# Optimization experiments

Hardware: AMD Instinct MI355X
Metric: run time of the kernel (lower is better)

The kernel has to match this reference:

```python
import jax, jax.numpy as jnp
import numpy as np

B, S, E, H, Dh = 2, 2048, 1024, 16, 64


def setup_inputs() -> dict:
    key = jax.random.key(0)
    ks = jax.random.split(key, 8)
    w = 0.02
    return {
        "x": jax.random.normal(ks[0], (B, S, E), jnp.float32),
        # torch Linear convention: weight (out, in) = (Dh, E), stacked over heads
        "Wq": jax.random.normal(ks[1], (H, Dh, E), jnp.float32) * w,
        "bq": jax.random.normal(ks[2], (H, Dh), jnp.float32) * w,
        "Wk": jax.random.normal(ks[3], (H, Dh, E), jnp.float32) * w,
        "bk": jax.random.normal(ks[4], (H, Dh), jnp.float32) * w,
        "Wv": jax.random.normal(ks[5], (H, Dh, E), jnp.float32) * w,
        "bv": jax.random.normal(ks[6], (H, Dh), jnp.float32) * w,
        "proj": jax.random.normal(ks[7], (H * Dh, E), jnp.float32) * w,
    }


def reference(x, Wq, bq, Wk, bk, Wv, bv, proj):
    b, s, e = x.shape
    h, dh, _ = Wq.shape
    scale = jnp.sqrt(jnp.asarray(dh, x.dtype))
    # per-head linear projections: y = x @ W.T + b  -> (b, h, s, dh)
    q = jnp.einsum('bse,hde->bhsd', x, Wq) + bq[None, :, None, :]
    k = jnp.einsum('bse,hde->bhsd', x, Wk) + bk[None, :, None, :]
    v = jnp.einsum('bse,hde->bhsd', x, Wv) + bv[None, :, None, :]
    causal = jnp.triu(jnp.ones((s, s), bool), 1)
    scores = jnp.einsum('bhsd,bhtd->bhst', q, k) / scale
    scores = jnp.where(causal[None, None], -jnp.inf, scores)
    # quirk: softmax output divided by sqrt(head_size) a second time
    att = jax.nn.softmax(scores, axis=-1) / scale
    z = jnp.einsum('bhst,bhtd->bhsd', att, v)
    # quirk: torch reshapes (B,H,S,Dh) row-major into (B,S,H*Dh) WITHOUT transpose
    z = z.reshape(b, s, h * dh)
    return z @ proj
```

## Files before the change

### kernel.cpp

```cpp
#include <hip/hip_runtime.h>
#include <hip/hip_bf16.h>

typedef unsigned short u16;
typedef unsigned int u32;
typedef __bf16 bf16x8 __attribute__((ext_vector_type(8)));
typedef float f32x4 __attribute__((ext_vector_type(4)));
typedef u16 u16x8 __attribute__((ext_vector_type(8)));
typedef u16 u16x4 __attribute__((ext_vector_type(4)));
typedef u32 u32x4 __attribute__((ext_vector_type(4)));

#define B_ 2
#define S_ 2048
#define E_ 1024
#define H_ 16
#define Dh_ 64

static __device__ __forceinline__ u16 f2bf(float f) {
  unsigned u = __builtin_bit_cast(unsigned, f);
  u += 0x7fff + ((u >> 16) & 1);
  return (u16)(u >> 16);
}

static __device__ __forceinline__ void gload16(const u16* g, u16* l) {
  __builtin_amdgcn_global_load_lds((const __attribute__((address_space(1))) unsigned int*)g,
                                   (__attribute__((address_space(3))) unsigned int*)l,
                                   16, 0, 0);
}

__global__ void cvt_all(const float* __restrict__ x, const float* __restrict__ wq,
                        const float* __restrict__ wk, const float* __restrict__ wv,
                        u16* __restrict__ xb, u16* __restrict__ wcat) {
  const int i = blockIdx.x * 256 + threadIdx.x;
  const float* src; u16x8* dst;
  if (i < 524288) {
    src = x + (size_t)i * 8;            dst = (u16x8*)xb + i;
  } else {
    const int j = i - 524288;
    dst = (u16x8*)wcat + j;
    if (j < 131072)      src = wq + (size_t)j * 8;
    else if (j < 262144) src = wk + (size_t)(j - 131072) * 8;
    else                 src = wv + (size_t)(j - 262144) * 8;
  }
  float4 a = ((const float4*)src)[0], b = ((const float4*)src)[1];
  u16x8 o;
  o[0] = f2bf(a.x); o[1] = f2bf(a.y); o[2] = f2bf(a.z); o[3] = f2bf(a.w);
  o[4] = f2bf(b.x); o[5] = f2bf(b.y); o[6] = f2bf(b.z); o[7] = f2bf(b.w);
  *dst = o;
}

__global__ void transpose_cvt(const float* __restrict__ in, u16* __restrict__ outT) {
  __shared__ float t[32][33];
  const int e = blockIdx.x * 32 + threadIdx.x;
  const int f = blockIdx.y * 32 + threadIdx.y;
  t[threadIdx.y][threadIdx.x] = in[f * 1024 + e];
  __syncthreads();
  const int eo = blockIdx.x * 32 + threadIdx.y;
  const int fo = blockIdx.y * 32 + threadIdx.x;
  outT[eo * 1024 + fo] = f2bf(t[threadIdx.x][threadIdx.y]);
}

__global__ __launch_bounds__(512, 2) void qkv_gemm(const u16* __restrict__ Wcat,
                                                   const u16* __restrict__ Xm,
                                                   const float* __restrict__ bq,
                                                   const float* __restrict__ bk,
                                                   const float* __restrict__ bv,
                                                   u16* __restrict__ Qb, u16* __restrict__ Kb,
                                                   u16* __restrict__ Vtb, float qs) {
  __shared__ __align__(16) u16 Alds[2][16384];
  __shared__ __align__(16) u16 Blds[2][16384];
  const int tid = threadIdx.x;
  const int wv = tid >> 6, ln = tid & 63;
  const int lq = ln & 15, lg = ln >> 4;
  const int wm = wv >> 2, wn = wv & 3;
  const int bid = blockIdx.x;
  const int xcd = bid & 7, w = bid >> 3;
  const int bx = w % 12;
  const int by = xcd * 2 + w / 12;
  const int ra0 = bx * 256, rb0 = by * 256;

  const int r_t = tid >> 3, c_t = tid & 7;
  const int gcol = (c_t ^ (r_t & 7)) * 8;
  const u16* Asrc = Wcat + (ra0 + r_t) * 1024 + gcol;
  const u16* Bsrc = Xm   + (rb0 + r_t) * 1024 + gcol;

  const int sc0 = (lg ^ (lq & 7)) * 8;
  const int sc1 = ((4 + lg) ^ (lq & 7)) * 8;
  const int baseA = (wm * 128 + lq) * 64;
  const int baseB = (wn * 64 + lq) * 64;

  f32x4 acc[8][4];
  const f32x4 z4 = {0.f, 0.f, 0.f, 0.f};
#pragma unroll
  for (int i = 0; i < 8; ++i)
#pragma unroll
    for (int j = 0; j < 4; ++j) acc[i][j] = z4;

#define SA(Q, KT, BUF) gload16(Asrc + (Q) * 65536 + (KT) * 64, &Alds[BUF][((Q) * 512 + tid) * 8])
#define SB(Q, KT, BUF) gload16(Bsrc + (Q) * 65536 + (KT) * 64, &Blds[BUF][((Q) * 512 + tid) * 8])
#define LOADA(MH, SC) do {                                                         \
    _Pragma("unroll") for (int ii = 0; ii < 4; ++ii)                               \
      af[ii] = *(const bf16x8*)&Alds[cb][baseA + (MH) * 4096 + ii * 1024 + (SC)];  \
  } while (0)
#define LOADB(DST, SC) do {                                                        \
    _Pragma("unroll") for (int j = 0; j < 4; ++j)                                  \
      DST[j] = *(const bf16x8*)&Blds[cb][baseB + j * 1024 + (SC)];                 \
  } while (0)
#define MF(MH, BQ) do {                                                            \
    _Pragma("unroll") for (int ii = 0; ii < 4; ++ii)                               \
      _Pragma("unroll") for (int j = 0; j < 4; ++j)                                \
        acc[(MH) * 4 + ii][j] =                                                    \
            __builtin_amdgcn_mfma_f32_16x16x32_bf16(af[ii], BQ[j],                 \
                                                    acc[(MH) * 4 + ii][j], 0, 0, 0); \
  } while (0)

  SB(0, 0, 0); SB(1, 0, 0); SB(2, 0, 0); SB(3, 0, 0);
  SA(0, 0, 0); SA(2, 0, 0); SA(1, 0, 0); SA(3, 0, 0);

  for (int kt = 0; kt < 16; ++kt) {
    const int cb = kt & 1, nb = cb ^ 1;
    const bool st = (kt < 15);
    asm volatile("s_waitcnt vmcnt(2)" ::: "memory");
    __builtin_amdgcn_s_barrier();
    __builtin_amdgcn_sched_barrier(0);
    bf16x8 af[4], bq0[4], bq1[4];
    LOADA(0, sc0);
    LOADB(bq0, sc0);
    if (st) { SB(0, kt + 1, nb); SB(1, kt + 1, nb); }
    __builtin_amdgcn_s_barrier();
    asm volatile("s_waitcnt lgkmcnt(0)" ::: "memory");
    __builtin_amdgcn_sched_barrier(0);
    __builtin_amdgcn_s_setprio(1);
    MF(0, bq0);
    __builtin_amdgcn_s_setprio(0);
    __builtin_amdgcn_s_barrier();
    LOADA(0, sc1);
    LOADB(bq1, sc1);
    if (st) { SB(2, kt + 1, nb); SB(3, kt + 1, nb); }
    __builtin_amdgcn_s_barrier();
    asm volatile("s_waitcnt lgkmcnt(0)" ::: "memory");
    __builtin_amdgcn_sched_barrier(0);
    __builtin_amdgcn_s_setprio(1);
    MF(0, bq1);
    __builtin_amdgcn_s_setprio(0);
    __builtin_amdgcn_s_barrier();
    if (st) { asm volatile("s_waitcnt vmcnt(4)" ::: "memory"); }
    else    { asm volatile("s_waitcnt vmcnt(0)" ::: "memory"); }
    __builtin_amdgcn_s_barrier();
    __builtin_amdgcn_sched_barrier(0);
    LOADA(1, sc0);
    if (st) { SA(0, kt + 1, nb); SA(2, kt + 1, nb); }
    __builtin_amdgcn_s_barrier();
    asm volatile("s_waitcnt lgkmcnt(0)" ::: "memory");
    __builtin_amdgcn_sched_barrier(0);
    __builtin_amdgcn_s_setprio(1);
    MF(1, bq0);
    __builtin_amdgcn_s_setprio(0);
    __builtin_amdgcn_s_barrier();
    LOADA(1, sc1);
    if (st) { SA(1, kt + 1, nb); SA(3, kt + 1, nb); }
    __builtin_amdgcn_s_barrier();
    asm volatile("s_waitcnt lgkmcnt(0)" ::: "memory");
    __builtin_amdgcn_sched_barrier(0);
    __builtin_amdgcn_s_setprio(1);
    MF(1, bq1);
    __builtin_amdgcn_s_setprio(0);
    __builtin_amdgcn_s_barrier();
  }
#undef SA
#undef SB
#undef LOADA
#undef LOADB
#undef MF

  const int region = bx >> 2;
  const float* bias = (region == 0) ? bq : (region == 1) ? bk : bv;
  const float osc = (region == 0) ? qs : 1.0f;
#pragma unroll
  for (int i = 0; i < 8; ++i) {
#pragma unroll
    for (int j = 0; j < 4; ++j) {
      const int n0 = ra0 + wm * 128 + (i >> 2) * 64 + (i & 3) * 16 + lg * 4;
      const int nl = n0 & 1023;
      const int h = nl >> 6, d = nl & 63;
      const int m = rb0 + wn * 64 + j * 16 + lq;
      const int bb = m >> 11, s = m & 2047;
      const float4 b4 = *(const float4*)&bias[nl];
      if (region < 2) {
        u16* out = (region == 0) ? Qb : Kb;
        u16x4 pk;
        pk[0] = f2bf((acc[i][j][0] + b4.x) * osc);
        pk[1] = f2bf((acc[i][j][1] + b4.y) * osc);
        pk[2] = f2bf((acc[i][j][2] + b4.z) * osc);
        pk[3] = f2bf((acc[i][j][3] + b4.w) * osc);
        *(u16x4*)&out[((bb * H_ + h) * S_ + s) * Dh_ + d] = pk;
      } else {
        const float bvv[4] = {b4.x, b4.y, b4.z, b4.w};
#pragma unroll
        for (int r = 0; r < 4; ++r)
          Vtb[((bb * H_ + h) * Dh_ + d + r) * S_ + s] = f2bf(acc[i][j][r] + bvv[r]);
      }
    }
  }
}

__global__ __launch_bounds__(256) void proj_gemm(const u16* __restrict__ Am,
                                                 const u16* __restrict__ Bm,
                                                 float* __restrict__ out) {
  __shared__ __align__(16) u16 As[2][4096];
  __shared__ __align__(16) u16 Bs[2][2048];
  const int tid = threadIdx.x;
  const int wv = tid >> 6, ln = tid & 63;
  const int lq = ln & 15, lg = ln >> 4;
  const int bid = blockIdx.x;
  const int xcd = bid & 7, within = bid >> 3;
  const int bx = within & 7;
  const int by = xcd * 8 + (within >> 3);
  const int ra0 = bx * 128, rb0 = by * 64;
  const int wra = wv >> 1, wrb = wv & 1;

  f32x4 acc[4][2];
  const f32x4 z4 = {0.f, 0.f, 0.f, 0.f};
#pragma unroll
  for (int i = 0; i < 4; ++i)
#pragma unroll
    for (int j = 0; j < 2; ++j) acc[i][j] = z4;

  const int arow = tid >> 2;
  const int acol = (tid & 3) * 8;
  const int brow = wv * 16 + (ln >> 2);
  const int bcol = (ln & 3) * 8;
  const u16* Ags = Am + (ra0 + arow) * 1024 + acol;
  const u16* Bgs = Bm + (rb0 + brow) * 1024 + bcol;

#define PSTAGE(KT, BUF) do { const int k0_ = (KT) * 32;              \
    gload16(Ags + k0_,         &As[BUF][wv * 512]);                  \
    gload16(Ags + 65536 + k0_, &As[BUF][wv * 512 + 2048]);           \
    gload16(Bgs + k0_,         &Bs[BUF][wv * 512]); } while (0)

  PSTAGE(0, 0);
  for (int kt = 0; kt < 32; ++kt) {
    const int cb = kt & 1;
    if (kt < 31) {
      PSTAGE(kt + 1, cb ^ 1);
      asm volatile("s_waitcnt vmcnt(3)" ::: "memory");
    } else {
      asm volatile("s_waitcnt vmcnt(0)" ::: "memory");
    }
    __builtin_amdgcn_s_barrier();
    __builtin_amdgcn_sched_barrier(0);
    bf16x8 af[4], bfr[2];
#pragma unroll
    for (int i = 0; i < 4; ++i)
      af[i] = *(const bf16x8*)&As[cb][(wra * 64 + i * 16 + lq) * 32 + lg * 8];
#pragma unroll
    for (int j = 0; j < 2; ++j)
      bfr[j] = *(const bf16x8*)&Bs[cb][(wrb * 32 + j * 16 + lq) * 32 + lg * 8];
#pragma unroll
    for (int i = 0; i < 4; ++i)
#pragma unroll
      for (int j = 0; j < 2; ++j)
        acc[i][j] = __builtin_amdgcn_mfma_f32_16x16x32_bf16(af[i], bfr[j], acc[i][j], 0, 0, 0);
    __builtin_amdgcn_sched_barrier(0);
    __builtin_amdgcn_s_barrier();
  }
#undef PSTAGE

  const int Ar = ra0 + wra * 64, Br = rb0 + wrb * 32;
#pragma unroll
  for (int i = 0; i < 4; ++i)
#pragma unroll
    for (int j = 0; j < 2; ++j) {
      const int e0 = Ar + i * 16 + lg * 4;
      const int m = Br + j * 16 + lq;
      *(f32x4*)&out[m * 1024 + e0] = acc[i][j];
    }
}

__global__ __launch_bounds__(512, 4) void attn_kernel(const u16* __restrict__ Q,
                                                      const u16* __restrict__ K,
                                                      const u16* __restrict__ Vt,
                                                      u16* __restrict__ Z) {
  __shared__ __align__(16) u16 Ktile[2][8192];
  __shared__ __align__(16) u16 Vtile[2][8192];
  const int tid = threadIdx.x;
  const int wv = tid >> 6, ln = tid & 63;
  const int lq = ln & 15, lg = ln >> 4;
  const bool lgodd = (lg & 1) != 0;
  const int id = blockIdx.x;
  const int within = id >> 3;
  const int xg = id & 7;
  int bh, qt;
  if (within < 32) { bh = xg * 4 + (within >> 4);     qt = 15 - (within & 15); }
  else { const int w = within - 32; bh = xg * 4 + 2 + (w >> 4); qt = w & 15; }
  const int qrow = (qt << 7) + wv * 16 + lq;
  const u16* Qp = Q + (size_t)bh * S_ * Dh_;
  const u16* Kp = K + (size_t)bh * S_ * Dh_;
  const u16* Vp = Vt + (size_t)bh * Dh_ * S_;

  int kgofs[2], vgrow[2], vgcol[2];
#pragma unroll
  for (int j = 0; j < 2; ++j) {
    const int p = j * 512 + tid;
    const int gk = p ^ ((p >> 3) & 7);
    kgofs[j] = (gk >> 3) * 64 + (gk & 7) * 8;
    vgrow[j] = p >> 4;
    vgcol[j] = ((p & 15) ^ ((p >> 4) & 15)) * 8;
  }
  const int sc0 = (lg ^ (lq & 7)) * 8;
  const int sc1 = ((4 + lg) ^ (lq & 7)) * 8;

  bf16x8 qf0 = *(const bf16x8*)&Qp[qrow * Dh_ + lg * 8];
  bf16x8 qf1 = *(const bf16x8*)&Qp[qrow * Dh_ + 32 + lg * 8];

  f32x4 o[4];
  const f32x4 z4 = {0.f, 0.f, 0.f, 0.f};
#pragma unroll
  for (int dt = 0; dt < 4; ++dt) o[dt] = z4;
  float l_lane = 0.f;

#define STAGE(KT, BUF) do { const int kb_ = (KT) * 128;                              \
    gload16(Kp + (size_t)kb_ * 64 + kgofs[0], &Ktile[BUF][wv * 512]);                \
    gload16(Kp + (size_t)kb_ * 64 + kgofs[1], &Ktile[BUF][4096 + wv * 512]);         \
    gload16(Vp + (size_t)vgrow[0] * 2048 + kb_ + vgcol[0], &Vtile[BUF][wv * 512]);   \
    gload16(Vp + (size_t)vgrow[1] * 2048 + kb_ + vgcol[1], &Vtile[BUF][4096 + wv * 512]); \
  } while (0)

  STAGE(0, 0);

  int cur = 0;
  for (int kt = 0; kt <= qt; ++kt) {
    if (kt < qt) {
      STAGE(kt + 1, cur ^ 1);
      asm volatile("s_waitcnt vmcnt(4)" ::: "memory");
    } else {
      asm volatile("s_waitcnt vmcnt(0)" ::: "memory");
    }
    __builtin_amdgcn_s_barrier();
    __builtin_amdgcn_sched_barrier(0);
    const int k0 = kt * 128;
    const bool diag = (kt == qt);
    const int nkk = diag ? ((wv >> 1) + 1) : 4;
#pragma unroll
    for (int kk = 0; kk < 4; ++kk) {
      if (kk < nkk) {
        const int rA = (kk * 32 + lq) * 64;
        const int rB = rA + 1024;
        bf16x8 kA0 = *(const bf16x8*)&Ktile[cur][rA + sc0];
        bf16x8 kA1 = *(const bf16x8*)&Ktile[cur][rA + sc1];
        bf16x8 kB0 = *(const bf16x8*)&Ktile[cur][rB + sc0];
        bf16x8 kB1 = *(const bf16x8*)&Ktile[cur][rB + sc1];
        f32x4 sa = z4, sb = z4;
        __builtin_amdgcn_s_setprio(1);
        sa = __builtin_amdgcn_mfma_f32_16x16x32_bf16(kA0, qf0, sa, 0, 0, 0);
        sa = __builtin_amdgcn_mfma_f32_16x16x32_bf16(kA1, qf1, sa, 0, 0, 0);
        sb = __builtin_amdgcn_mfma_f32_16x16x32_bf16(kB0, qf0, sb, 0, 0, 0);
        sb = __builtin_amdgcn_mfma_f32_16x16x32_bf16(kB1, qf1, sb, 0, 0, 0);
        __builtin_amdgcn_s_setprio(0);
        if (diag) {
          const int keyA = k0 + kk * 32 + lg * 4;
          const int keyB = keyA + 16;
#pragma unroll
          for (int r = 0; r < 4; ++r) {
            if (keyA + r > qrow) sa[r] = -3.0e38f;
            if (keyB + r > qrow) sb[r] = -3.0e38f;
          }
        }
        float e0 = __builtin_amdgcn_exp2f(sa[0]);
        float e1 = __builtin_amdgcn_exp2f(sa[1]);
        float e2 = __builtin_amdgcn_exp2f(sa[2]);
        float e3 = __builtin_amdgcn_exp2f(sa[3]);
        float f0 = __builtin_amdgcn_exp2f(sb[0]);
        float f1 = __builtin_amdgcn_exp2f(sb[1]);
        float f2 = __builtin_amdgcn_exp2f(sb[2]);
        float f3 = __builtin_amdgcn_exp2f(sb[3]);
        l_lane += ((e0 + e1) + (e2 + e3)) + ((f0 + f1) + (f2 + f3));
        u32 A0, A1, B0, B1;
        asm("v_cvt_pk_bf16_f32 %0, %1, %2" : "=v"(A0) : "v"(e0), "v"(e1));
        asm("v_cvt_pk_bf16_f32 %0, %1, %2" : "=v"(A1) : "v"(e2), "v"(e3));
        asm("v_cvt_pk_bf16_f32 %0, %1, %2" : "=v"(B0) : "v"(f0), "v"(f1));
        asm("v_cvt_pk_bf16_f32 %0, %1, %2" : "=v"(B1) : "v"(f2), "v"(f3));
        asm("v_permlane32_swap_b32 %0, %1" : "+v"(A0), "+v"(B0));
        asm("v_permlane32_swap_b32 %0, %1" : "+v"(A1), "+v"(B1));
        const u32 A0x = __shfl_xor((int)A0, 16), B0x = __shfl_xor((int)B0, 16);
        const u32 A1x = __shfl_xor((int)A1, 16), B1x = __shfl_xor((int)B1, 16);
        u32x4 w;
        w[0] = lgodd ? B0x : A0;
        w[1] = lgodd ? B1x : A1;
        w[2] = lgodd ? B0 : A0x;
        w[3] = lgodd ? B1 : A1x;
        const bf16x8 pf = __builtin_bit_cast(bf16x8, w);
        const int scvk = ((kk * 4 + lg) ^ lq) * 8;
        __builtin_amdgcn_s_setprio(1);
#pragma unroll
        for (int dt = 0; dt < 4; ++dt) {
          bf16x8 vf = *(const bf16x8*)&Vtile[cur][(dt * 16 + lq) * 128 + scvk];
          o[dt] = __builtin_amdgcn_mfma_f32_16x16x32_bf16(vf, pf, o[dt], 0, 0, 0);
        }
        __builtin_amdgcn_s_setprio(0);
      }
    }
    __builtin_amdgcn_sched_barrier(0);
    __builtin_amdgcn_s_barrier();
    cur ^= 1;
  }
#undef STAGE

  float l = l_lane;
  l += __shfl_xor(l, 16);
  l += __shfl_xor(l, 32);
  const float inv = 0.125f / l;
#pragma unroll
  for (int dt = 0; dt < 4; ++dt) {
    u16x4 pko;
#pragma unroll
    for (int r = 0; r < 4; ++r) pko[r] = f2bf(o[dt][r] * inv);
    *(u16x4*)&Z[((size_t)bh * S_ + qrow) * Dh_ + dt * 16 + lg * 4] = pko;
  }
}

extern "C" void kernel_launch(void* const* d_in, const int* in_sizes, int n_in,
                              void* d_out, int out_size, void* d_ws, size_t ws_size,
                              hipStream_t stream) {
  const float* x    = (const float*)d_in[0];
  const float* Wq   = (const float*)d_in[1];
  const float* bq   = (const float*)d_in[2];
  const float* Wk   = (const float*)d_in[3];
  const float* bk   = (const float*)d_in[4];
  const float* Wv   = (const float*)d_in[5];
  const float* bv   = (const float*)d_in[6];
  const float* proj = (const float*)d_in[7];
  float* out = (float*)d_out;

  char* p = (char*)d_ws;
  u16* xb   = (u16*)p; p += (size_t)4096 * 1024 * 2;
  u16* wcat = (u16*)p; p += (size_t)3072 * 1024 * 2;
  u16* pjt  = (u16*)p; p += (size_t)1024 * 1024 * 2;
  u16* Qb   = (u16*)p; p += (size_t)4096 * 1024 * 2;
  u16* Kb   = (u16*)p; p += (size_t)4096 * 1024 * 2;
  u16* Vtb  = (u16*)p; p += (size_t)4096 * 1024 * 2;
  u16* Zb   = (u16*)p; p += (size_t)4096 * 1024 * 2;

  cvt_all<<<dim3(3584), dim3(256), 0, stream>>>(x, Wq, Wk, Wv, xb, wcat);
  transpose_cvt<<<dim3(32, 32), dim3(32, 32), 0, stream>>>(proj, pjt);

  const float qs = 0.125f * 1.44269504f;
  qkv_gemm<<<dim3(192), dim3(512), 0, stream>>>(wcat, xb, bq, bk, bv, Qb, Kb, Vtb, qs);

  attn_kernel<<<dim3(512), dim3(512), 0, stream>>>(Qb, Kb, Vtb, Zb);

  proj_gemm<<<dim3(512), dim3(256), 0, stream>>>(pjt, Zb, out);
}
```

Before: 104.6 us.

## Merge proj transpose into convert kernel and use one barrier per K-step

Folds the proj transpose-and-convert into the cvt_all launch as extra blocks, which saves one kernel launch. In the proj GEMM and attention loops, the code now waits for all loads and hits one barrier before issuing the next stage's prefetch, dropping the trailing barrier. The proj GEMM MFMAs also get raised priority. This removes a barrier per iteration, but the prefetch is issued later and vmcnt(0) waits for everything, which may reduce how much load latency the double buffer hides.

```diff
diff --git a/kernel.cpp b/kernel.cpp
--- a/kernel.cpp
+++ b/kernel.cpp
@@ -29,34 +29,44 @@
 
 __global__ void cvt_all(const float* __restrict__ x, const float* __restrict__ wq,
                         const float* __restrict__ wk, const float* __restrict__ wv,
-                        u16* __restrict__ xb, u16* __restrict__ wcat) {
-  const int i = blockIdx.x * 256 + threadIdx.x;
-  const float* src; u16x8* dst;
-  if (i < 524288) {
-    src = x + (size_t)i * 8;            dst = (u16x8*)xb + i;
+                        const float* __restrict__ proj,
+                        u16* __restrict__ xb, u16* __restrict__ wcat, u16* __restrict__ pjt) {
+  __shared__ float tt[32][33];
+  const int bid = blockIdx.x;
+  const int tid = threadIdx.x;
+  if (bid < 3584) {
+    const int i = bid * 256 + tid;
+    const float* src; u16x8* dst;
+    if (i < 524288) {
+      src = x + (size_t)i * 8;            dst = (u16x8*)xb + i;
+    } else {
+      const int j = i - 524288;
+      dst = (u16x8*)wcat + j;
+      if (j < 131072)      src = wq + (size_t)j * 8;
+      else if (j < 262144) src = wk + (size_t)(j - 131072) * 8;
+      else                 src = wv + (size_t)(j - 262144) * 8;
+    }
+    float4 a = ((const float4*)src)[0], b = ((const float4*)src)[1];
+    u16x8 o;
+    o[0] = f2bf(a.x); o[1] = f2bf(a.y); o[2] = f2bf(a.z); o[3] = f2bf(a.w);
+    o[4] = f2bf(b.x); o[5] = f2bf(b.y); o[6] = f2bf(b.z); o[7] = f2bf(b.w);
+    *dst = o;
   } else {
-    const int j = i - 524288;
-    dst = (u16x8*)wcat + j;
-    if (j < 131072)      src = wq + (size_t)j * 8;
-    else if (j < 262144) src = wk + (size_t)(j - 131072) * 8;
-    else                 src = wv + (size_t)(j - 262144) * 8;
-  }
-  float4 a = ((const float4*)src)[0], b = ((const float4*)src)[1];
-  u16x8 o;
-  o[0] = f2bf(a.x); o[1] = f2bf(a.y); o[2] = f2bf(a.z); o[3] = f2bf(a.w);
-  o[4] = f2bf(b.x); o[5] = f2bf(b.y); o[6] = f2bf(b.z); o[7] = f2bf(b.w);
-  *dst = o;
-}
-
-__global__ void transpose_cvt(const float* __restrict__ in, u16* __restrict__ outT) {
-  __shared__ float t[32][33];
-  const int e = blockIdx.x * 32 + threadIdx.x;
-  const int f = blockIdx.y * 32 + threadIdx.y;
-  t[threadIdx.y][threadIdx.x] = in[f * 1024 + e];
-  __syncthreads();
-  const int eo = blockIdx.x * 32 + threadIdx.y;
-  const int fo = blockIdx.y * 32 + threadIdx.x;
-  outT[eo * 1024 + fo] = f2bf(t[threadIdx.x][threadIdx.y]);
+    const int tb = bid - 3584;
+    const int e0 = (tb & 31) * 32, f0 = (tb >> 5) * 32;
+    const int tx = tid & 31, ty = tid >> 5;
+#pragma unroll
+    for (int r = 0; r < 4; ++r) {
+      const int row = ty + r * 8;
+      tt[row][tx] = proj[(f0 + row) * 1024 + e0 + tx];
+    }
+    __syncthreads();
+#pragma unroll
+    for (int r = 0; r < 4; ++r) {
+      const int row = ty + r * 8;
+      pjt[(e0 + row) * 1024 + f0 + tx] = f2bf(tt[tx][row]);
+    }
+  }
 }
 
 __global__ __launch_bounds__(512, 2) void qkv_gemm(const u16* __restrict__ Wcat,
@@ -240,14 +250,10 @@
   PSTAGE(0, 0);
   for (int kt = 0; kt < 32; ++kt) {
     const int cb = kt & 1;
-    if (kt < 31) {
-      PSTAGE(kt + 1, cb ^ 1);
-      asm volatile("s_waitcnt vmcnt(3)" ::: "memory");
-    } else {
-      asm volatile("s_waitcnt vmcnt(0)" ::: "memory");
-    }
-    __builtin_amdgcn_s_barrier();
-    __builtin_amdgcn_sched_barrier(0);
+    asm volatile("s_waitcnt vmcnt(0)" ::: "memory");
+    __builtin_amdgcn_s_barrier();
+    __builtin_amdgcn_sched_barrier(0);
+    if (kt < 31) PSTAGE(kt + 1, cb ^ 1);
     bf16x8 af[4], bfr[2];
 #pragma unroll
     for (int i = 0; i < 4; ++i)
@@ -255,13 +261,13 @@
 #pragma unroll
     for (int j = 0; j < 2; ++j)
       bfr[j] = *(const bf16x8*)&Bs[cb][(wrb * 32 + j * 16 + lq) * 32 + lg * 8];
+    __builtin_amdgcn_s_setprio(1);
 #pragma unroll
     for (int i = 0; i < 4; ++i)
 #pragma unroll
       for (int j = 0; j < 2; ++j)
         acc[i][j] = __builtin_amdgcn_mfma_f32_16x16x32_bf16(af[i], bfr[j], acc[i][j], 0, 0, 0);
-    __builtin_amdgcn_sched_barrier(0);
-    __builtin_amdgcn_s_barrier();
+    __builtin_amdgcn_s_setprio(0);
   }
 #undef PSTAGE
 
@@ -329,14 +335,10 @@
 
   int cur = 0;
   for (int kt = 0; kt <= qt; ++kt) {
-    if (kt < qt) {
-      STAGE(kt + 1, cur ^ 1);
-      asm volatile("s_waitcnt vmcnt(4)" ::: "memory");
-    } else {
-      asm volatile("s_waitcnt vmcnt(0)" ::: "memory");
-    }
-    __builtin_amdgcn_s_barrier();
-    __builtin_amdgcn_sched_barrier(0);
+    asm volatile("s_waitcnt vmcnt(0)" ::: "memory");
+    __builtin_amdgcn_s_barrier();
+    __builtin_amdgcn_sched_barrier(0);
+    if (kt < qt) STAGE(kt + 1, cur ^ 1);
     const int k0 = kt * 128;
     const bool diag = (kt == qt);
     const int nkk = diag ? ((wv >> 1) + 1) : 4;
@@ -399,8 +401,6 @@
         __builtin_amdgcn_s_setprio(0);
       }
     }
-    __builtin_amdgcn_sched_barrier(0);
-    __builtin_amdgcn_s_barrier();
     cur ^= 1;
   }
 #undef STAGE
@@ -440,8 +440,7 @@
   u16* Vtb  = (u16*)p; p += (size_t)4096 * 1024 * 2;
   u16* Zb   = (u16*)p; p += (size_t)4096 * 1024 * 2;
 
-  cvt_all<<<dim3(3584), dim3(256), 0, stream>>>(x, Wq, Wk, Wv, xb, wcat);
-  transpose_cvt<<<dim3(32, 32), dim3(32, 32), 0, stream>>>(proj, pjt);
+  cvt_all<<<dim3(4608), dim3(256), 0, stream>>>(x, Wq, Wk, Wv, proj, xb, wcat, pjt);
 
   const float qs = 0.125f * 1.44269504f;
   qkv_gemm<<<dim3(192), dim3(512), 0, stream>>>(wcat, xb, bq, bk, bv, Qb, Kb, Vtb, qs);
```

Measured after the change: 101.2 us. 1.03x faster.
